# Kernel tuning notes

Measured on AMD Instinct MI355X. Metric: run time of the kernel, lower is better.

Reference implementation:

```python
import jax, jax.numpy as jnp
import numpy as np

B = 64
SEQ = 192
LABEL = 48
PRED = 168
DEC_LEN = LABEL + PRED  # 216
ENC_IN = 7
DEC_IN = 7
C_OUT = 7
MARK = 4
D_MODEL = 1024
E_LAYERS = 2
D_LAYERS = 2


def setup_inputs() -> dict:
    key = jax.random.key(0)
    keys = iter(jax.random.split(key, 64))
    s = 1.0 / np.sqrt(D_MODEL)

    def u(shape):
        return jax.random.uniform(next(keys), shape, jnp.float32, -s, s)

    inp = {
        "x_enc": jax.random.normal(next(keys), (B, SEQ, ENC_IN), jnp.float32),
        "x_mark_enc": jax.random.normal(next(keys), (B, SEQ, MARK), jnp.float32),
        "x_dec": jax.random.normal(next(keys), (B, DEC_LEN, DEC_IN), jnp.float32),
        "x_mark_dec": jax.random.normal(next(keys), (B, DEC_LEN, MARK), jnp.float32),
    }
    for pfx, nl, in0 in (("enc", E_LAYERS, ENC_IN + MARK), ("dec", D_LAYERS, DEC_IN + MARK)):
        for l in range(nl):
            d_in = in0 if l == 0 else D_MODEL
            inp[f"{pfx}_W_ih_l{l}"] = u((3 * D_MODEL, d_in))
            inp[f"{pfx}_W_hh_l{l}"] = u((3 * D_MODEL, D_MODEL))
            inp[f"{pfx}_b_ih_l{l}"] = u((3 * D_MODEL,))
            inp[f"{pfx}_b_hh_l{l}"] = u((3 * D_MODEL,))
    inp["out_W"] = u((C_OUT, D_MODEL))
    inp["out_b"] = u((C_OUT,))
    return inp


def _gru_cell(x, h, W_ih, W_hh, b_ih, b_hh):
    # torch gate order: r, z, n
    gi = x @ W_ih.T + b_ih   # [B, 3H]
    gh = h @ W_hh.T + b_hh   # [B, 3H]
    i_r, i_z, i_n = jnp.split(gi, 3, axis=-1)
    h_r, h_z, h_n = jnp.split(gh, 3, axis=-1)
    r = jax.nn.sigmoid(i_r + h_r)
    z = jax.nn.sigmoid(i_z + h_z)
    n = jnp.tanh(i_n + r * h_n)
    return (1.0 - z) * n + z * h


def _stack_step(layers, h_layers, x_t):
    # layers: list of (W_ih, W_hh, b_ih, b_hh); h_layers: [L, B, H]
    inp = x_t
    new_h = []
    for l, (W_ih, W_hh, b_ih, b_hh) in enumerate(layers):
        hn = _gru_cell(inp, h_layers[l], W_ih, W_hh, b_ih, b_hh)
        new_h.append(hn)
        inp = hn
    return jnp.stack(new_h, axis=0), inp  # new hidden stack, top-layer output


def _forward(x_enc, x_mark_enc, x_dec, x_mark_dec, enc_layers, dec_layers, out_W, out_b):
    xe = jnp.concatenate([x_enc, x_mark_enc], axis=-1)  # [B, S, enc_in+4]
    xd = jnp.concatenate([x_dec, x_mark_dec], axis=-1)  # [B, T, dec_in+4]

    # --- encoder: multilayer GRU, keep only final hidden state ---
    h0 = jnp.zeros((E_LAYERS, B, D_MODEL), xe.dtype)

    def enc_step(h, x_t):
        h_new, _ = _stack_step(enc_layers, h, x_t)
        return h_new, None

    h_enc, _ = jax.lax.scan(enc_step, h0, jnp.swapaxes(xe, 0, 1))  # xs: [S, B, D]

    xd_t = jnp.swapaxes(xd, 0, 1)  # [T, B, dec_in+4]
    ts = jnp.arange(DEC_LEN)

    def dec_step(carry, xs):
        h, prev = carry
        x_t, t = xs
        marks = x_t[:, -MARK:]
        auto_in = jnp.concatenate([prev, marks], axis=-1)  # needs dec_in == c_out
        inp = jnp.where(t < LABEL, x_t, auto_in)
        h_new, out = _stack_step(dec_layers, h, inp)
        pred = out @ out_W.T + out_b  # [B, c_out]
        return (h_new, pred), pred

    prev0 = jnp.zeros((B, C_OUT), xd.dtype)
    _, preds = jax.lax.scan(dec_step, (h_enc, prev0), (xd_t, ts))  # [T, B, c_out]
    preds = jnp.swapaxes(preds, 0, 1)  # [B, T, c_out]
    return preds[:, -PRED:, :]


def reference(x_enc, x_mark_enc, x_dec, x_mark_dec,
              enc_W_ih_l0, enc_W_hh_l0, enc_b_ih_l0, enc_b_hh_l0,
              enc_W_ih_l1, enc_W_hh_l1, enc_b_ih_l1, enc_b_hh_l1,
              dec_W_ih_l0, dec_W_hh_l0, dec_b_ih_l0, dec_b_hh_l0,
              dec_W_ih_l1, dec_W_hh_l1, dec_b_ih_l1, dec_b_hh_l1,
              out_W, out_b):
    enc_layers = [
        (enc_W_ih_l0, enc_W_hh_l0, enc_b_ih_l0, enc_b_hh_l0),
        (enc_W_ih_l1, enc_W_hh_l1, enc_b_ih_l1, enc_b_hh_l1),
    ]
    dec_layers = [
        (dec_W_ih_l0, dec_W_hh_l0, dec_b_ih_l0, dec_b_hh_l0),
        (dec_W_ih_l1, dec_W_hh_l1, dec_b_ih_l1, dec_b_hh_l1),
    ]
    return _forward(x_enc, x_mark_enc, x_dec, x_mark_dec, enc_layers, dec_layers, out_W, out_b)
```

## Files before the change

### kernel.cpp

```cpp
#include <hip/hip_runtime.h>
#include <math.h>


typedef _Float16 half8 __attribute__((ext_vector_type(8)));
typedef _Float16 half4f __attribute__((ext_vector_type(4)));
typedef float f32x4 __attribute__((ext_vector_type(4)));

#define DM    1024
#define TENC  192
#define TDEC  216
#define LBL   48
#define NPRED 168
#define HB    131072
#define HE    65536

#define OFF_H0P0 8192
#define OFF_EH10 (OFF_H0P0 + 2*HB)
#define OFF_DH1  (OFF_EH10 + 2*HB)
#define OFF_WF   (OFF_DH1 + 217*HB)
#define OFF_BF0  (OFF_WF + 3072*1024*2)

#define L_TA0 0
#define L_TA1 32768
#define L_TB0 65536
#define L_TB1 98304
#define L_XW  131072
#define L_BA  131648
#define L_BAA 131712
#define L_BB  131776
#define L_TRA 131840
#define L_TRB 140032
#define L_HSTA 148224
#define L_HSTB 148736
#define SMEM_BYTES 149248

__device__ __forceinline__ float sigm(float x) { return 1.0f / (1.0f + __expf(-x)); }

__device__ __forceinline__ void coh_store64(void* p, unsigned long long v) {
  asm volatile("global_store_dwordx2 %0, %1, off sc0 sc1" :: "v"(p), "v"(v) : "memory");
}
__device__ __forceinline__ unsigned coh_load32(const void* p) {
  unsigned r;
  asm volatile("global_load_dword %0, %1, off sc0 sc1\n\ts_waitcnt vmcnt(0)"
               : "=v"(r) : "v"(p) : "memory");
  return r;
}
__device__ __forceinline__ half8 coh_load_h8(const void* p) {
  half8 r;
  asm volatile("global_load_dwordx4 %0, %1, off sc0 sc1" : "=v"(r) : "v"(p));
  return r;
}
__device__ __forceinline__ void ysync16(half8* y) {
  asm volatile("s_waitcnt vmcnt(0)"
               : "+v"(y[0]), "+v"(y[1]), "+v"(y[2]), "+v"(y[3]),
                 "+v"(y[4]), "+v"(y[5]), "+v"(y[6]), "+v"(y[7]),
                 "+v"(y[8]), "+v"(y[9]), "+v"(y[10]), "+v"(y[11]),
                 "+v"(y[12]), "+v"(y[13]), "+v"(y[14]), "+v"(y[15])
               :: "memory");
}

__device__ __forceinline__ void bar_arrive(unsigned* leaf, unsigned* root,
                                           int tid, int bx, unsigned ep) {
  asm volatile("s_waitcnt vmcnt(0)" ::: "memory");
  __syncthreads();
  if (tid == 0) {
    unsigned old = __hip_atomic_fetch_add(&leaf[(bx >> 3) << 5], 1u,
                                          __ATOMIC_RELAXED, __HIP_MEMORY_SCOPE_AGENT);
    if (old == ep * 8u - 1u)
      __hip_atomic_fetch_add(root, 1u, __ATOMIC_RELAXED, __HIP_MEMORY_SCOPE_AGENT);
  }
}
__device__ __forceinline__ void bar_wait(unsigned* root, int tid, unsigned ep) {
  if (tid == 0) {
    while (coh_load32(root) < ep * 32u) __builtin_amdgcn_s_sleep(1);
  }
  __syncthreads();
}

__device__ __forceinline__ void fill_tile_f32(char* smem, int off, const float* __restrict__ src,
                                              int u0, int g0, int g1, int g2, int g3, int tid) {
  const int w = tid >> 6, lane = tid & 63;
  int gsel[4] = {g0, g1, g2, g3};
#pragma unroll
  for (int mm = 0; mm < 2; ++mm) {
    const int m = w + mm * 8;
    const int g = gsel[m >> 2];
    const long srow = (g < 0) ? -1 : (long)g * DM + u0 + (m & 3);
#pragma unroll
    for (int p = 0; p < 4; ++p) {
      const int k = p * 256 + lane * 4;
      half4f hv;
      if (srow >= 0) {
        float4 v = *(const float4*)(src + srow * DM + k);
        hv = (half4f){(_Float16)v.x, (_Float16)v.y, (_Float16)v.z, (_Float16)v.w};
      } else {
        hv = (half4f){(_Float16)0.f, (_Float16)0.f, (_Float16)0.f, (_Float16)0.f};
      }
      const int kb = k >> 5, q = (k >> 3) & 3;
      const int elem = (kb * 64 + q * 16 + m) * 8 + (k & 7);
      *(half4f*)(smem + off + elem * 2) = hv;
    }
  }
}

__device__ __forceinline__ void fill_tile_f16(char* smem, int off, const _Float16* __restrict__ src,
                                              int u0, int g0, int g1, int g2, int g3, int tid) {
  const int w = tid >> 6, lane = tid & 63;
  int gsel[4] = {g0, g1, g2, g3};
#pragma unroll
  for (int mm = 0; mm < 2; ++mm) {
    const int m = w + mm * 8;
    const int g = gsel[m >> 2];
    const long srow = (g < 0) ? -1 : (long)g * DM + u0 + (m & 3);
#pragma unroll
    for (int p = 0; p < 4; ++p) {
      const int k = p * 256 + lane * 4;
      half4f hv;
      if (srow >= 0) hv = *(const half4f*)(src + srow * DM + k);
      else hv = (half4f){(_Float16)0.f, (_Float16)0.f, (_Float16)0.f, (_Float16)0.f};
      const int kb = k >> 5, q = (k >> 3) & 3;
      const int elem = (kb * 64 + q * 16 + m) * 8 + (k & 7);
      *(half4f*)(smem + off + elem * 2) = hv;
    }
  }
}

__device__ __forceinline__ void fill_small(char* smem, int u0, int tid,
    const float* __restrict__ Wih0, const float* __restrict__ bihA, const float* __restrict__ bhhA,
    const float* __restrict__ bih1, const float* __restrict__ bhh1, const float* __restrict__ bf0) {
  if (tid < 132) {
    const int rr = tid / 11, c = tid - rr * 11;
    const int g = rr >> 2, ul = rr & 3;
    ((float*)(smem + L_XW))[(g * 4 + ul) * 12 + c] = Wih0[(g * DM + u0 + ul) * 11 + c];
  }
  if (tid < 4) {
    const int u = u0 + tid;
    float* bA = (float*)(smem + L_BA);
    bA[tid] = bihA[u] + bhhA[u];
    bA[4 + tid] = bihA[DM + u] + bhhA[DM + u];
    bA[8 + tid] = bhhA[2 * DM + u];
    bA[12 + tid] = bihA[2 * DM + u];
    float* bB = (float*)(smem + L_BB);
    bB[tid] = bih1[u] + bhh1[u];
    bB[4 + tid] = bih1[DM + u] + bhh1[DM + u];
    bB[8 + tid] = bhh1[2 * DM + u];
    bB[12 + tid] = bih1[2 * DM + u];
    if (bf0) {
      float* bAa = (float*)(smem + L_BAA);
      bAa[tid] = bf0[u] + bhhA[u];
      bAa[4 + tid] = bf0[DM + u] + bhhA[DM + u];
      bAa[8 + tid] = bhhA[2 * DM + u];
      bAa[12 + tid] = bf0[2 * DM + u];
    }
  }
}

#define MFMA16 __builtin_amdgcn_mfma_f32_16x16x32_f16
#define ZERO4 ((f32x4){0.f, 0.f, 0.f, 0.f})

__device__ __forceinline__ void yload(half8* y, const _Float16* src, int kb0, int lane, int bs) {
  const half8* B = (const half8*)src + ((lane >> 4) << 6) + bs + (lane & 15);
#pragma unroll
  for (int i = 0; i < 16; ++i)
    y[i] = coh_load_h8(B + ((size_t)(kb0 + i) << 8));
}

__device__ __forceinline__ f32x4 gemm_reg(const char* smem, int toff, int kb0, int lane,
                                          const half8* y, f32x4 seed) {
  const half8* T = (const half8*)(smem + toff);
  f32x4 aE = seed, aO = ZERO4;
#pragma unroll
  for (int i = 0; i < 16; i += 2) {
    aE = MFMA16(T[((kb0 + i) << 6) + lane], y[i], aE, 0, 0, 0);
    aO = MFMA16(T[((kb0 + i + 1) << 6) + lane], y[i + 1], aO, 0, 0, 0);
  }
  return aE + aO;
}

__device__ __forceinline__ void tr_store(char* smem, int trOff, int w, int lane, f32x4 acc) {
  float* tr = (float*)(smem + trOff) + (w << 8);
  const int quad = lane >> 4, col = lane & 15;
  tr[(quad * 4 + 0) * 16 + col] = acc[0];
  tr[(quad * 4 + 1) * 16 + col] = acc[1];
  tr[(quad * 4 + 2) * 16 + col] = acc[2];
  tr[(quad * 4 + 3) * 16 + col] = acc[3];
}

__device__ __forceinline__ void x_pre(const char* smem, int xmode,
    const float* __restrict__ xin, const float* __restrict__ xmk,
    int t, int seqT, int b, int ul, float& xr, float& xz, float& xn) {
  const float* xw = (const float*)(smem + L_XW);
  xr = 0.f; xz = 0.f; xn = 0.f;
  if (xmode == 1) {
    const float* xp = xin + (size_t)(b * seqT + t) * 7;
#pragma unroll
    for (int c = 0; c < 7; ++c) {
      float v = xp[c];
      xr = fmaf(xw[ul * 12 + c], v, xr);
      xz = fmaf(xw[(4 + ul) * 12 + c], v, xz);
      xn = fmaf(xw[(8 + ul) * 12 + c], v, xn);
    }
  }
  const float* mp = xmk + (size_t)(b * seqT + t) * 4;
#pragma unroll
  for (int m = 0; m < 4; ++m) {
    float v = mp[m];
    xr = fmaf(xw[ul * 12 + 7 + m], v, xr);
    xz = fmaf(xw[(4 + ul) * 12 + 7 + m], v, xz);
    xn = fmaf(xw[(8 + ul) * 12 + 7 + m], v, xn);
  }
}

__device__ __forceinline__ void epi(char* smem, int trOff, int stOff, int wb,
                                    int biasOff, float pxr, float pxz, float pxn,
                                    int tid, float& hprev) {
  const int lane = tid & 63, w = tid >> 6;
  const int bg = w - wb;
  const int col = lane & 15, ul = lane >> 4;
  const float* t0 = (const float*)(smem + trOff) + (bg << 8);
  const float* t1 = t0 + (4 << 8);
  const int b = (bg << 4) + col;
  float vr  = t0[ul * 16 + col]        + t1[ul * 16 + col];
  float vz  = t0[(4 + ul) * 16 + col]  + t1[(4 + ul) * 16 + col];
  float vnh = t0[(8 + ul) * 16 + col]  + t1[(8 + ul) * 16 + col];
  float vni = t0[(12 + ul) * 16 + col] + t1[(12 + ul) * 16 + col];
  const float* bias = (const float*)(smem + biasOff);
  float rg = sigm(vr + bias[ul] + pxr);
  float zg = sigm(vz + bias[4 + ul] + pxz);
  float ng = tanhf((vni + bias[12 + ul] + pxn) + rg * (vnh + bias[8 + ul]));
  float hn = ng + zg * (hprev - ng);
  hprev = hn;
  ((_Float16*)(smem + stOff))[b * 4 + ul] = (_Float16)hn;
}

__device__ __forceinline__ void st8(_Float16* dst, int u0, int i, const char* stage) {
  unsigned long long v = *(const unsigned long long*)(stage + i * 8);
  char* gp = (char*)dst + (((size_t)(u0 >> 3)) * 64 + i) * 16 + (size_t)(u0 & 7) * 2;
  coh_store64(gp, v);
}

__global__ __launch_bounds__(256) void prep_wf(const float* __restrict__ dWih0,
                                               const float* __restrict__ dbih0,
                                               const float* __restrict__ outW,
                                               const float* __restrict__ outb,
                                               char* __restrict__ ws) {
  const int j = blockIdx.x;
  _Float16* wf = (_Float16*)(ws + OFF_WF);
  float* bf0 = (float*)(ws + OFF_BF0);
  float wrow[7];
#pragma unroll
  for (int c = 0; c < 7; ++c) wrow[c] = dWih0[j * 11 + c];
#pragma unroll
  for (int p = 0; p < 4; ++p) {
    const int k = p * 256 + threadIdx.x;
    float acc = 0.f;
#pragma unroll
    for (int c = 0; c < 7; ++c) acc = fmaf(wrow[c], outW[c * DM + k], acc);
    wf[(size_t)j * DM + k] = (_Float16)acc;
  }
  if (threadIdx.x == 0) {
    float bb = dbih0[j];
#pragma unroll
    for (int c = 0; c < 7; ++c) bb = fmaf(wrow[c], outb[c], bb);
    bf0[j] = bb;
  }
}

__global__ __launch_bounds__(512) void gru_persist(
    const float* __restrict__ xe,  const float* __restrict__ xme,
    const float* __restrict__ xd,  const float* __restrict__ xmd,
    const float* __restrict__ eWih0, const float* __restrict__ eWhh0,
    const float* __restrict__ ebih0, const float* __restrict__ ebhh0,
    const float* __restrict__ eWih1, const float* __restrict__ eWhh1,
    const float* __restrict__ ebih1, const float* __restrict__ ebhh1,
    const float* __restrict__ dWih0, const float* __restrict__ dWhh0,
    const float* __restrict__ dbih0, const float* __restrict__ dbhh0,
    const float* __restrict__ dWih1, const float* __restrict__ dWhh1,
    const float* __restrict__ dbih1, const float* __restrict__ dbhh1,
    char* __restrict__ ws) {
  extern __shared__ char smem[];
  const int tid = threadIdx.x, bx = blockIdx.x;
  const int lane = tid & 63;
  const int w = tid >> 6;
  const int bg = w & 3, kslice = w >> 2;
  const int bs = bg << 4, kb0 = kslice << 4;
  const int u0 = bx << 2;
  const int bA = ((w & 3) << 4) + (lane & 15);
  const int ulA = lane >> 4;

  unsigned* leaf = (unsigned*)ws;
  unsigned* root = (unsigned*)(ws + 4096);
  _Float16* h0p[2] = {(_Float16*)(ws + OFF_H0P0), (_Float16*)(ws + OFF_H0P0 + HB)};
  _Float16* eh1[2] = {(_Float16*)(ws + OFF_EH10), (_Float16*)(ws + OFF_EH10 + HB)};
  _Float16* dh1 = (_Float16*)(ws + OFF_DH1);
  const _Float16* wf = (const _Float16*)(ws + OFF_WF);
  const float* bf0 = (const float*)(ws + OFF_BF0);

  half8 y0[16], y1[16];
  f32x4 carryI = ZERO4, carryA = ZERO4, carryB = ZERO4;
  float pxr = 0.f, pxz = 0.f, pxn = 0.f;
  float hA = 0.f, hB = 0.f;
  unsigned ep = 0;

  fill_tile_f32(smem, L_TA0, eWhh0, u0, 0, 1, 2, -1, tid);
  fill_tile_f32(smem, L_TB0, eWih1, u0, 0, 1, -1, 2, tid);
  fill_tile_f32(smem, L_TB1, eWhh1, u0, 0, 1, 2, -1, tid);
  fill_small(smem, u0, tid, eWih0, ebih0, ebhh0, ebih1, ebhh1, nullptr);
  __syncthreads();
  if (w < 4) x_pre(smem, 1, xe, xme, 0, TENC, bA, ulA, pxr, pxz, pxn);

  for (int t = 0; t < TENC; ++t) {
    bar_wait(root, tid, ep);
    yload(y0, h0p[t & 1], kb0, lane, bs);
    if (t >= 2) yload(y1, eh1[(t - 3) & 1], kb0, lane, bs);
    ysync16(y0);
    f32x4 aA = gemm_reg(smem, L_TA0, kb0, lane, y0, ZERO4);
    tr_store(smem, L_TRA, w, lane, aA);
    if (t >= 2) {
      f32x4 aB = gemm_reg(smem, L_TB1, kb0, lane, y1, carryI);
      tr_store(smem, L_TRB, w, lane, aB);
    }
    __syncthreads();
    if (w < 4) epi(smem, L_TRA, L_HSTA, 0, L_BA, pxr, pxz, pxn, tid, hA);
    else if (t >= 2) epi(smem, L_TRB, L_HSTB, 4, L_BB, 0.f, 0.f, 0.f, tid, hB);
    __syncthreads();
    if (tid < 64) st8(h0p[(t & 1) ^ 1], u0, tid, smem + L_HSTA);
    else if (t >= 2 && tid < 128) st8(eh1[t & 1], u0, tid - 64, smem + L_HSTB);
    bar_arrive(leaf, root, tid, bx, ++ep);
    carryI = gemm_reg(smem, L_TB0, kb0, lane, y0, ZERO4);
    if (w < 4 && t + 1 < TENC) x_pre(smem, 1, xe, xme, t + 1, TENC, bA, ulA, pxr, pxz, pxn);
  }
  {
    bar_wait(root, tid, ep);
    yload(y0, h0p[0], kb0, lane, bs);
    yload(y1, eh1[1], kb0, lane, bs);
    ysync16(y0);
    f32x4 aB = gemm_reg(smem, L_TB1, kb0, lane, y1, carryI);
    tr_store(smem, L_TRB, w, lane, aB);
    __syncthreads();
    if (w >= 4) epi(smem, L_TRB, L_HSTB, 4, L_BB, 0.f, 0.f, 0.f, tid, hB);
    __syncthreads();
    if (tid >= 64 && tid < 128) st8(eh1[0], u0, tid - 64, smem + L_HSTB);
    bar_arrive(leaf, root, tid, bx, ++ep);
    carryI = gemm_reg(smem, L_TB0, kb0, lane, y0, ZERO4);
  }
  {
    bar_wait(root, tid, ep);
    yload(y1, eh1[0], kb0, lane, bs);
    ysync16(y1);
    f32x4 aB = gemm_reg(smem, L_TB1, kb0, lane, y1, carryI);
    tr_store(smem, L_TRB, w, lane, aB);
    __syncthreads();
    if (w >= 4) epi(smem, L_TRB, L_HSTB, 4, L_BB, 0.f, 0.f, 0.f, tid, hB);
    __syncthreads();
    if (tid >= 64 && tid < 128) st8(dh1, u0, tid - 64, smem + L_HSTB);
    bar_arrive(leaf, root, tid, bx, ++ep);
    fill_tile_f32(smem, L_TA0, dWhh0, u0, 0, 1, 2, -1, tid);
    fill_tile_f16(smem, L_TA1, wf,    u0, 0, 1, -1, 2, tid);
    fill_tile_f32(smem, L_TB0, dWih1, u0, 0, 1, -1, 2, tid);
    fill_tile_f32(smem, L_TB1, dWhh1, u0, 0, 1, 2, -1, tid);
    fill_small(smem, u0, tid, dWih0, dbih0, dbhh0, dbih1, dbhh1, bf0);
    __syncthreads();
    if (w < 4) x_pre(smem, 1, xd, xmd, 0, TDEC, bA, ulA, pxr, pxz, pxn);
  }

  for (int d = 0; d < LBL; ++d) {
    bar_wait(root, tid, ep);
    yload(y0, h0p[d & 1], kb0, lane, bs);
    if (d >= 2) yload(y1, dh1 + (size_t)(d - 2) * HE, kb0, lane, bs);
    ysync16(y0);
    f32x4 aA = gemm_reg(smem, L_TA0, kb0, lane, y0, ZERO4);
    tr_store(smem, L_TRA, w, lane, aA);
    if (d >= 2) {
      f32x4 aB = gemm_reg(smem, L_TB1, kb0, lane, y1, carryI);
      tr_store(smem, L_TRB, w, lane, aB);
    }
    __syncthreads();
    if (w < 4) epi(smem, L_TRA, L_HSTA, 0, L_BA, pxr, pxz, pxn, tid, hA);
    else if (d >= 2) epi(smem, L_TRB, L_HSTB, 4, L_BB, 0.f, 0.f, 0.f, tid, hB);
    __syncthreads();
    if (tid < 64) st8(h0p[(d & 1) ^ 1], u0, tid, smem + L_HSTA);
    else if (d >= 2 && tid < 128) st8(dh1 + (size_t)(d - 1) * HE, u0, tid - 64, smem + L_HSTB);
    bar_arrive(leaf, root, tid, bx, ++ep);
    carryI = gemm_reg(smem, L_TB0, kb0, lane, y0, ZERO4);
    if (w < 4 && d + 1 < LBL) x_pre(smem, 1, xd, xmd, d + 1, TDEC, bA, ulA, pxr, pxz, pxn);
  }
  {
    bar_wait(root, tid, ep);
    yload(y0, h0p[0], kb0, lane, bs);
    yload(y1, dh1 + (size_t)46 * HE, kb0, lane, bs);
    ysync16(y0);
    f32x4 aB = gemm_reg(smem, L_TB1, kb0, lane, y1, carryI);
    tr_store(smem, L_TRB, w, lane, aB);
    __syncthreads();
    if (w >= 4) epi(smem, L_TRB, L_HSTB, 4, L_BB, 0.f, 0.f, 0.f, tid, hB);
    __syncthreads();
    if (tid >= 64 && tid < 128) st8(dh1 + (size_t)47 * HE, u0, tid - 64, smem + L_HSTB);
    bar_arrive(leaf, root, tid, bx, ++ep);
    carryI = gemm_reg(smem, L_TB0, kb0, lane, y0, ZERO4);
    carryA = gemm_reg(smem, L_TA0, kb0, lane, y0, ZERO4);
  }
  {
    bar_wait(root, tid, ep);
    yload(y1, dh1 + (size_t)47 * HE, kb0, lane, bs);
    ysync16(y1);
    f32x4 aB = gemm_reg(smem, L_TB1, kb0, lane, y1, carryI);
    tr_store(smem, L_TRB, w, lane, aB);
    __syncthreads();
    if (w >= 4) epi(smem, L_TRB, L_HSTB, 4, L_BB, 0.f, 0.f, 0.f, tid, hB);
    __syncthreads();
    if (tid >= 64 && tid < 128) st8(dh1 + (size_t)48 * HE, u0, tid - 64, smem + L_HSTB);
    bar_arrive(leaf, root, tid, bx, ++ep);
    if (w < 4) x_pre(smem, 2, nullptr, xmd, LBL, TDEC, bA, ulA, pxr, pxz, pxn);
  }

  for (int s = LBL; s < TDEC; ++s) {
    bar_wait(root, tid, ep);
    yload(y1, dh1 + (size_t)s * HE, kb0, lane, bs);
    ysync16(y1);
    f32x4 aA = gemm_reg(smem, L_TA1, kb0, lane, y1, carryA);
    tr_store(smem, L_TRA, w, lane, aA);
    __syncthreads();
    if (w < 4) epi(smem, L_TRA, L_HSTA, 0, L_BAA, pxr, pxz, pxn, tid, hA);
    __syncthreads();
    if (tid < 64) st8(h0p[(s & 1) ^ 1], u0, tid, smem + L_HSTA);
    bar_arrive(leaf, root, tid, bx, ++ep);
    carryB = gemm_reg(smem, L_TB1, kb0, lane, y1, ZERO4);
    bar_wait(root, tid, ep);
    yload(y0, h0p[(s & 1) ^ 1], kb0, lane, bs);
    ysync16(y0);
    f32x4 aB = gemm_reg(smem, L_TB0, kb0, lane, y0, carryB);
    tr_store(smem, L_TRB, w, lane, aB);
    __syncthreads();
    if (w >= 4) epi(smem, L_TRB, L_HSTB, 4, L_BB, 0.f, 0.f, 0.f, tid, hB);
    __syncthreads();
    if (tid >= 64 && tid < 128) st8(dh1 + (size_t)(s + 1) * HE, u0, tid - 64, smem + L_HSTB);
    bar_arrive(leaf, root, tid, bx, ++ep);
    carryA = gemm_reg(smem, L_TA0, kb0, lane, y0, ZERO4);
    if (w < 4 && s + 1 < TDEC) x_pre(smem, 2, nullptr, xmd, s + 1, TDEC, bA, ulA, pxr, pxz, pxn);
  }
}

__global__ __launch_bounds__(64) void proj_kernel(const char* __restrict__ ws,
                                                  const float* __restrict__ outW,
                                                  const float* __restrict__ outb,
                                                  float* __restrict__ out) {
  const int ti = blockIdx.x / 7, c = blockIdx.x % 7;
  const _Float16* h = (const _Float16*)(ws + OFF_DH1) + (size_t)(LBL + 1 + ti) * HE;
  const int b = threadIdx.x;
  const float* wrow = outW + c * DM;
  float acc = outb[c];
#pragma unroll 4
  for (int k8 = 0; k8 < 128; ++k8) {
    const half8 hv = *(const half8*)(h + ((size_t)k8 * 64 + b) * 8);
    const float* wp = wrow + k8 * 8;
#pragma unroll
    for (int j = 0; j < 8; ++j) acc = fmaf((float)hv[j], wp[j], acc);
  }
  out[(size_t)b * (NPRED * 7) + ti * 7 + c] = acc;
}

extern "C" void kernel_launch(void* const* d_in, const int* in_sizes, int n_in,
                              void* d_out, int out_size, void* d_ws, size_t ws_size,
                              hipStream_t stream) {
  (void)in_sizes; (void)n_in; (void)out_size; (void)ws_size;
  const float* xe    = (const float*)d_in[0];
  const float* xme   = (const float*)d_in[1];
  const float* xd    = (const float*)d_in[2];
  const float* xmd   = (const float*)d_in[3];
  const float* eWih0 = (const float*)d_in[4];
  const float* eWhh0 = (const float*)d_in[5];
  const float* ebih0 = (const float*)d_in[6];
  const float* ebhh0 = (const float*)d_in[7];
  const float* eWih1 = (const float*)d_in[8];
  const float* eWhh1 = (const float*)d_in[9];
  const float* ebih1 = (const float*)d_in[10];
  const float* ebhh1 = (const float*)d_in[11];
  const float* dWih0 = (const float*)d_in[12];
  const float* dWhh0 = (const float*)d_in[13];
  const float* dbih0 = (const float*)d_in[14];
  const float* dbhh0 = (const float*)d_in[15];
  const float* dWih1 = (const float*)d_in[16];
  const float* dWhh1 = (const float*)d_in[17];
  const float* dbih1 = (const float*)d_in[18];
  const float* dbhh1 = (const float*)d_in[19];
  const float* outW  = (const float*)d_in[20];
  const float* outb  = (const float*)d_in[21];
  char* ws = (char*)d_ws;

  hipFuncSetAttribute(reinterpret_cast<const void*>(gru_persist),
                      hipFuncAttributeMaxDynamicSharedMemorySize, SMEM_BYTES);

  hipMemsetAsync(ws, 0, OFF_H0P0 + HB, stream);
  hipMemsetAsync(ws + OFF_EH10, 0, 2 * HB, stream);

  prep_wf<<<3072, 256, 0, stream>>>(dWih0, dbih0, outW, outb, ws);
  gru_persist<<<256, 512, SMEM_BYTES, stream>>>(xe, xme, xd, xmd,
                                                eWih0, eWhh0, ebih0, ebhh0,
                                                eWih1, eWhh1, ebih1, ebhh1,
                                                dWih0, dWhh0, dbih0, dbhh0,
                                                dWih1, dWhh1, dbih1, dbhh1, ws);
  proj_kernel<<<NPRED * 7, 64, 0, stream>>>(ws, outW, outb, (float*)d_out);
}
```

Measured before the change: 3.067 ms.

## Replace global tree barrier with per-wave waits on only the needed leaf counters

Removes the root counter of the two-level grid barrier. Each wave now polls only the 16 leaf counters covering the k-slice of hidden state it will load, and proceeds once those blocks have arrived. This shortens the critical path by dropping the second atomic hop and the block-wide syncthreads after the wait, so waves can start as soon as their dependencies are ready. In exchange many more lanes spin on coherent loads without sleeping, which adds memory traffic, and the correctness of partial synchronisation depends on the reuse distance of the ping-pong buffers.

After: 2.816 ms. 8.2% less time.

```diff
diff --git a/kernel.cpp b/kernel.cpp
--- a/kernel.cpp
+++ b/kernel.cpp
@@ -59,22 +59,17 @@
                :: "memory");
 }
 
-__device__ __forceinline__ void bar_arrive(unsigned* leaf, unsigned* root,
-                                           int tid, int bx, unsigned ep) {
+__device__ __forceinline__ void bar_arrive(unsigned* leaf, int tid, int bx) {
   asm volatile("s_waitcnt vmcnt(0)" ::: "memory");
   __syncthreads();
-  if (tid == 0) {
-    unsigned old = __hip_atomic_fetch_add(&leaf[(bx >> 3) << 5], 1u,
-                                          __ATOMIC_RELAXED, __HIP_MEMORY_SCOPE_AGENT);
-    if (old == ep * 8u - 1u)
-      __hip_atomic_fetch_add(root, 1u, __ATOMIC_RELAXED, __HIP_MEMORY_SCOPE_AGENT);
-  }
-}
-__device__ __forceinline__ void bar_wait(unsigned* root, int tid, unsigned ep) {
-  if (tid == 0) {
-    while (coh_load32(root) < ep * 32u) __builtin_amdgcn_s_sleep(1);
-  }
-  __syncthreads();
+  if (tid == 0)
+    __hip_atomic_fetch_add(&leaf[(bx >> 3) << 5], 1u,
+                           __ATOMIC_RELAXED, __HIP_MEMORY_SCOPE_AGENT);
+}
+__device__ __forceinline__ void wave_wait(unsigned* leaf, int lane, int kb0, unsigned ep) {
+  const unsigned tgt = ep * 8u;
+  const unsigned* p = &leaf[(unsigned)(kb0 + (lane & 15)) << 5];
+  while (!__all((int)(coh_load32(p) >= tgt))) { }
 }
 
 __device__ __forceinline__ void fill_tile_f32(char* smem, int off, const float* __restrict__ src,
@@ -289,7 +284,6 @@
   const int ulA = lane >> 4;
 
   unsigned* leaf = (unsigned*)ws;
-  unsigned* root = (unsigned*)(ws + 4096);
   _Float16* h0p[2] = {(_Float16*)(ws + OFF_H0P0), (_Float16*)(ws + OFF_H0P0 + HB)};
   _Float16* eh1[2] = {(_Float16*)(ws + OFF_EH10), (_Float16*)(ws + OFF_EH10 + HB)};
   _Float16* dh1 = (_Float16*)(ws + OFF_DH1);
@@ -310,7 +304,7 @@
   if (w < 4) x_pre(smem, 1, xe, xme, 0, TENC, bA, ulA, pxr, pxz, pxn);
 
   for (int t = 0; t < TENC; ++t) {
-    bar_wait(root, tid, ep);
+    wave_wait(leaf, lane, kb0, ep);
     yload(y0, h0p[t & 1], kb0, lane, bs);
     if (t >= 2) yload(y1, eh1[(t - 3) & 1], kb0, lane, bs);
     ysync16(y0);
@@ -326,12 +320,12 @@
     __syncthreads();
     if (tid < 64) st8(h0p[(t & 1) ^ 1], u0, tid, smem + L_HSTA);
     else if (t >= 2 && tid < 128) st8(eh1[t & 1], u0, tid - 64, smem + L_HSTB);
-    bar_arrive(leaf, root, tid, bx, ++ep);
+    bar_arrive(leaf, tid, bx); ++ep;
     carryI = gemm_reg(smem, L_TB0, kb0, lane, y0, ZERO4);
     if (w < 4 && t + 1 < TENC) x_pre(smem, 1, xe, xme, t + 1, TENC, bA, ulA, pxr, pxz, pxn);
   }
   {
-    bar_wait(root, tid, ep);
+    wave_wait(leaf, lane, kb0, ep);
     yload(y0, h0p[0], kb0, lane, bs);
     yload(y1, eh1[1], kb0, lane, bs);
     ysync16(y0);
@@ -341,11 +335,11 @@
     if (w >= 4) epi(smem, L_TRB, L_HSTB, 4, L_BB, 0.f, 0.f, 0.f, tid, hB);
     __syncthreads();
     if (tid >= 64 && tid < 128) st8(eh1[0], u0, tid - 64, smem + L_HSTB);
-    bar_arrive(leaf, root, tid, bx, ++ep);
+    bar_arrive(leaf, tid, bx); ++ep;
     carryI = gemm_reg(smem, L_TB0, kb0, lane, y0, ZERO4);
   }
   {
-    bar_wait(root, tid, ep);
+    wave_wait(leaf, lane, kb0, ep);
     yload(y1, eh1[0], kb0, lane, bs);
     ysync16(y1);
     f32x4 aB = gemm_reg(smem, L_TB1, kb0, lane, y1, carryI);
@@ -354,7 +348,7 @@
     if (w >= 4) epi(smem, L_TRB, L_HSTB, 4, L_BB, 0.f, 0.f, 0.f, tid, hB);
     __syncthreads();
     if (tid >= 64 && tid < 128) st8(dh1, u0, tid - 64, smem + L_HSTB);
-    bar_arrive(leaf, root, tid, bx, ++ep);
+    bar_arrive(leaf, tid, bx); ++ep;
     fill_tile_f32(smem, L_TA0, dWhh0, u0, 0, 1, 2, -1, tid);
     fill_tile_f16(smem, L_TA1, wf,    u0, 0, 1, -1, 2, tid);
     fill_tile_f32(smem, L_TB0, dWih1, u0, 0, 1, -1, 2, tid);
@@ -365,7 +359,7 @@
   }
 
   for (int d = 0; d < LBL; ++d) {
-    bar_wait(root, tid, ep);
+    wave_wait(leaf, lane, kb0, ep);
     yload(y0, h0p[d & 1], kb0, lane, bs);
     if (d >= 2) yload(y1, dh1 + (size_t)(d - 2) * HE, kb0, lane, bs);
     ysync16(y0);
@@ -381,12 +375,12 @@
     __syncthreads();
     if (tid < 64) st8(h0p[(d & 1) ^ 1], u0, tid, smem + L_HSTA);
     else if (d >= 2 && tid < 128) st8(dh1 + (size_t)(d - 1) * HE, u0, tid - 64, smem + L_HSTB);
-    bar_arrive(leaf, root, tid, bx, ++ep);
+    bar_arrive(leaf, tid, bx); ++ep;
     carryI = gemm_reg(smem, L_TB0, kb0, lane, y0, ZERO4);
     if (w < 4 && d + 1 < LBL) x_pre(smem, 1, xd, xmd, d + 1, TDEC, bA, ulA, pxr, pxz, pxn);
   }
   {
-    bar_wait(root, tid, ep);
+    wave_wait(leaf, lane, kb0, ep);
     yload(y0, h0p[0], kb0, lane, bs);
     yload(y1, dh1 + (size_t)46 * HE, kb0, lane, bs);
     ysync16(y0);
@@ -396,12 +390,12 @@
     if (w >= 4) epi(smem, L_TRB, L_HSTB, 4, L_BB, 0.f, 0.f, 0.f, tid, hB);
     __syncthreads();
     if (tid >= 64 && tid < 128) st8(dh1 + (size_t)47 * HE, u0, tid - 64, smem + L_HSTB);
-    bar_arrive(leaf, root, tid, bx, ++ep);
+    bar_arrive(leaf, tid, bx); ++ep;
     carryI = gemm_reg(smem, L_TB0, kb0, lane, y0, ZERO4);
     carryA = gemm_reg(smem, L_TA0, kb0, lane, y0, ZERO4);
   }
   {
-    bar_wait(root, tid, ep);
+    wave_wait(leaf, lane, kb0, ep);
     yload(y1, dh1 + (size_t)47 * HE, kb0, lane, bs);
     ysync16(y1);
     f32x4 aB = gemm_reg(smem, L_TB1, kb0, lane, y1, carryI);
@@ -410,12 +404,12 @@
     if (w >= 4) epi(smem, L_TRB, L_HSTB, 4, L_BB, 0.f, 0.f, 0.f, tid, hB);
     __syncthreads();
     if (tid >= 64 && tid < 128) st8(dh1 + (size_t)48 * HE, u0, tid - 64, smem + L_HSTB);
-    bar_arrive(leaf, root, tid, bx, ++ep);
+    bar_arrive(leaf, tid, bx); ++ep;
     if (w < 4) x_pre(smem, 2, nullptr, xmd, LBL, TDEC, bA, ulA, pxr, pxz, pxn);
   }
 
   for (int s = LBL; s < TDEC; ++s) {
-    bar_wait(root, tid, ep);
+    wave_wait(leaf, lane, kb0, ep);
     yload(y1, dh1 + (size_t)s * HE, kb0, lane, bs);
     ysync16(y1);
     f32x4 aA = gemm_reg(smem, L_TA1, kb0, lane, y1, carryA);
@@ -424,9 +418,9 @@
     if (w < 4) epi(smem, L_TRA, L_HSTA, 0, L_BAA, pxr, pxz, pxn, tid, hA);
     __syncthreads();
     if (tid < 64) st8(h0p[(s & 1) ^ 1], u0, tid, smem + L_HSTA);
-    bar_arrive(leaf, root, tid, bx, ++ep);
+    bar_arrive(leaf, tid, bx); ++ep;
     carryB = gemm_reg(smem, L_TB1, kb0, lane, y1, ZERO4);
-    bar_wait(root, tid, ep);
+    wave_wait(leaf, lane, kb0, ep);
     yload(y0, h0p[(s & 1) ^ 1], kb0, lane, bs);
     ysync16(y0);
     f32x4 aB = gemm_reg(smem, L_TB0, kb0, lane, y0, carryB);
@@ -435,7 +429,7 @@
     if (w >= 4) epi(smem, L_TRB, L_HSTB, 4, L_BB, 0.f, 0.f, 0.f, tid, hB);
     __syncthreads();
     if (tid >= 64 && tid < 128) st8(dh1 + (size_t)(s + 1) * HE, u0, tid - 64, smem + L_HSTB);
-    bar_arrive(leaf, root, tid, bx, ++ep);
+    bar_arrive(leaf, tid, bx); ++ep;
     carryA = gemm_reg(smem, L_TA0, kb0, lane, y0, ZERO4);
     if (w < 4 && s + 1 < TDEC) x_pre(smem, 2, nullptr, xmd, s + 1, TDEC, bA, ulA, pxr, pxz, pxn);
   }
```
